# Performance work log

Measured on AMD Instinct MI355X. Metric: run time of the kernel, lower is better.

## Reference

```python
import jax, jax.numpy as jnp
import numpy as np

N = 50000
H = 8
D = 32
E = 400000
IN = 128
NEG_SLOPE = 0.2


def _gat(h, edges, W, al, ar, b):
    # DGL GATConv: fc -> per-head attention logits -> edge softmax over dst -> aggregate
    src, dst = edges[0], edges[1]
    feat = (h @ W).reshape(N, H, D)                      # [N,H,D]
    el = jnp.einsum('nhd,hd->nh', feat, al)              # [N,H]
    er = jnp.einsum('nhd,hd->nh', feat, ar)              # [N,H]
    e = jax.nn.leaky_relu(el[src] + er[dst], NEG_SLOPE)  # [E,H]
    m = jax.ops.segment_max(e, dst, num_segments=N)      # [N,H] per-dst max
    m = jnp.where(jnp.isfinite(m), m, 0.0)
    m = jax.lax.stop_gradient(m)
    ex = jnp.exp(e - m[dst])                             # [E,H]
    denom = jax.ops.segment_sum(ex, dst, num_segments=N) # [N,H]
    alpha = ex / denom[dst]                              # edge softmax
    out = jax.ops.segment_sum(feat[src] * alpha[:, :, None], dst, num_segments=N)  # [N,H,D]
    return (out + b.reshape(1, H, D)).reshape(N, H * D)


def setup_inputs() -> dict:
    key = jax.random.key(0)
    ks = jax.random.split(key, 12)
    s = 0.05
    return {
        'h': jax.random.normal(ks[0], (N, IN), jnp.float32),
        'edges0': jax.random.randint(ks[1], (2, E), 0, N, jnp.int32),
        'edges1': jax.random.randint(ks[2], (2, E), 0, N, jnp.int32),
        'fc0': jax.random.normal(ks[3], (IN, H * D), jnp.float32) * s,
        'al0': jax.random.normal(ks[4], (H, D), jnp.float32) * s,
        'ar0': jax.random.normal(ks[5], (H, D), jnp.float32) * s,
        'bias0': jnp.zeros((H * D,), jnp.float32),
        'fc1': jax.random.normal(ks[6], (IN, H * D), jnp.float32) * s,
        'al1': jax.random.normal(ks[7], (H, D), jnp.float32) * s,
        'ar1': jax.random.normal(ks[8], (H, D), jnp.float32) * s,
        'bias1': jnp.zeros((H * D,), jnp.float32),
        'sw1': jax.random.normal(ks[9], (H * D, 128), jnp.float32) * s,
        'sb1': jnp.zeros((128,), jnp.float32),
        'sw2': jax.random.normal(ks[10], (128, 1), jnp.float32) * s,
    }


def reference(h, edges0, edges1, fc0, al0, ar0, bias0, fc1, al1, ar1, bias1, sw1, sb1, sw2):
    z0 = _gat(h, edges0, fc0, al0, ar0, bias0)   # [N, H*D]
    z1 = _gat(h, edges1, fc1, al1, ar1, bias1)   # [N, H*D]
    z = jnp.stack([z0, z1], axis=1)              # [N, M=2, H*D]
    # semantic attention: MLP -> mean over nodes -> softmax over meta-paths
    w = jnp.tanh(z @ sw1 + sb1) @ sw2            # [N,M,1]
    beta = jax.nn.softmax(w.mean(axis=0), axis=0)  # [M,1]
    return (beta[None] * z).sum(axis=1)          # [N, H*D]
```

## Files before the change

kernel.cpp:

```cpp
#include <hip/hip_runtime.h>
#include <math.h>

#define NEG_SLOPE 0.2f

typedef unsigned int uint;
typedef unsigned short ushort;
typedef __bf16 bf16x8 __attribute__((ext_vector_type(8)));
typedef float f32x4 __attribute__((ext_vector_type(4)));

__device__ __forceinline__ uint bf16r(float a) {
    uint u = __float_as_uint(a);
    return (u + 0x7fffu + ((u >> 16) & 1u)) >> 16;
}
__device__ __forceinline__ uint bf16pack(float a, float b) {
    return bf16r(a) | (bf16r(b) << 16);
}
__device__ __forceinline__ float bflo(uint u) { return __uint_as_float(u << 16); }
__device__ __forceinline__ float bfhi(uint u) { return __uint_as_float(u & 0xffff0000u); }

__global__ void prep_kernel(const float* __restrict__ fc0, const float* __restrict__ fc1,
                            const float* __restrict__ sw1, ushort* __restrict__ wbt,
                            ushort* __restrict__ sw1t, float* __restrict__ wsum) {
    int b = blockIdx.x;
    if (b == 0 && threadIdx.x == 0) { wsum[0] = 0.f; wsum[1] = 0.f; }
    if (b < 256) {
        int idx = b * 256 + threadIdx.x;
        const float* W = (idx >> 15) ? fc1 : fc0;
        int r = idx & 32767;
        int c = r >> 7, k = r & 127;
        wbt[idx] = (ushort)bf16r(W[(size_t)k * 256 + c]);
    } else {
        int idx = (b - 256) * 256 + threadIdx.x;
        int c = idx >> 8, p = idx & 255;
        int col = (p & ~63) + ((p & 3) * 16) + ((p >> 2) & 15);
        sw1t[idx] = (ushort)bf16r(sw1[(size_t)col * 128 + c]);
    }
}

__global__ void zero_counts_kernel(int* __restrict__ count, int* __restrict__ cursor, int Ntot) {
    int i = blockIdx.x * blockDim.x + threadIdx.x;
    if (i < Ntot) { count[i] = 0; cursor[i] = 0; }
}

__global__ void hist_kernel(const int* __restrict__ e0, const int* __restrict__ e1,
                            int* __restrict__ count, int E, int N) {
    int e = blockIdx.x * blockDim.x + threadIdx.x;
    if (e >= 2 * E) return;
    int l = (e >= E);
    int ee = e - l * E;
    const int* edges = l ? e1 : e0;
    atomicAdd(&count[edges[E + ee] + l * N], 1);
}

__global__ void scan1_kernel(const int* __restrict__ count, int* __restrict__ base,
                             int* __restrict__ bsum, int Ntot) {
    __shared__ int ws_s[4];
    int b = blockIdx.x;
    int i = b * 256 + threadIdx.x;
    int v = (i < Ntot) ? count[i] : 0;
    int lane = threadIdx.x & 63;
    int wid = threadIdx.x >> 6;
    int x = v;
#pragma unroll
    for (int s = 1; s < 64; s <<= 1) {
        int y = __shfl_up(x, s, 64);
        if (lane >= s) x += y;
    }
    if (lane == 63) ws_s[wid] = x;
    __syncthreads();
    int add = 0;
    for (int w = 0; w < wid; w++) add += ws_s[w];
    int incl = x + add;
    if (i < Ntot) base[i] = incl - v;
    if (threadIdx.x == 255) bsum[b] = incl;
}

__global__ void scan2_kernel(int* __restrict__ bsum, int nb) {
    __shared__ int ws_s[4];
    __shared__ int running_s;
    if (threadIdx.x == 0) running_s = 0;
    __syncthreads();
    int lane = threadIdx.x & 63;
    int wid = threadIdx.x >> 6;
    for (int c0 = 0; c0 < nb; c0 += 256) {
        int i = c0 + threadIdx.x;
        int v = (i < nb) ? bsum[i] : 0;
        int x = v;
#pragma unroll
        for (int s = 1; s < 64; s <<= 1) {
            int y = __shfl_up(x, s, 64);
            if (lane >= s) x += y;
        }
        if (lane == 63) ws_s[wid] = x;
        __syncthreads();
        int add = 0;
        for (int w = 0; w < wid; w++) add += ws_s[w];
        int incl = x + add;
        int run = running_s;
        if (i < nb) bsum[i] = run + incl - v;
        __syncthreads();
        if (threadIdx.x == 255) running_s = run + incl;
        __syncthreads();
    }
}

#define HKPAD 136
__global__ void __launch_bounds__(256, 4)
fc_kernel(const float* __restrict__ h, const ushort* __restrict__ wbt,
          const float* __restrict__ al0, const float* __restrict__ ar0,
          const float* __restrict__ al1, const float* __restrict__ ar1,
          ushort* __restrict__ featb, float* __restrict__ el,
          float* __restrict__ er, int N, int nb) {
    __shared__ ushort hs[64 * HKPAD];
    int b = blockIdx.x;
    int l = (b >= nb);
    int n0 = (b - l * nb) * 64;
    for (int t = threadIdx.x; t < 64 * 32; t += 256) {
        int r = t >> 5, i4 = t & 31;
        int n = n0 + r;
        float4 v = make_float4(0.f, 0.f, 0.f, 0.f);
        if (n < N) v = ((const float4*)h)[(size_t)n * 32 + i4];
        uint2 pk;
        pk.x = bf16pack(v.x, v.y);
        pk.y = bf16pack(v.z, v.w);
        *((uint2*)(hs + r * HKPAD + i4 * 4)) = pk;
    }
    __syncthreads();

    const ushort* wb = wbt + l * 32768;
    const float* al = l ? al1 : al0;
    const float* ar = l ? ar1 : ar0;
    ushort* fb = featb + (size_t)l * N * 256;
    float* elp = el + (size_t)l * N * 8;
    float* erp = er + (size_t)l * N * 8;

    int wv = threadIdx.x >> 6;
    int lane = threadIdx.x & 63;
    int lhi = lane >> 4, llo = lane & 15;

    f32x4 acc[4][4];
#pragma unroll
    for (int cb = 0; cb < 4; cb++)
#pragma unroll
        for (int rt = 0; rt < 4; rt++) acc[cb][rt] = (f32x4){0.f, 0.f, 0.f, 0.f};

#pragma unroll
    for (int ks = 0; ks < 4; ks++) {
        bf16x8 a[4];
#pragma unroll
        for (int rt = 0; rt < 4; rt++)
            a[rt] = *(const bf16x8*)(hs + (rt * 16 + llo) * HKPAD + ks * 32 + lhi * 8);
#pragma unroll
        for (int cb = 0; cb < 4; cb++) {
            bf16x8 bfrag = *(const bf16x8*)(wb + (size_t)(64 * wv + 16 * cb + llo) * 128 + ks * 32 + lhi * 8);
#pragma unroll
            for (int rt = 0; rt < 4; rt++)
                acc[cb][rt] = __builtin_amdgcn_mfma_f32_16x16x32_bf16(a[rt], bfrag, acc[cb][rt], 0, 0, 0);
        }
    }

    float alv0 = al[64 * wv + llo],      alv1 = al[64 * wv + 16 + llo];
    float alv2 = al[64 * wv + 32 + llo], alv3 = al[64 * wv + 48 + llo];
    float arv0 = ar[64 * wv + llo],      arv1 = ar[64 * wv + 16 + llo];
    float arv2 = ar[64 * wv + 32 + llo], arv3 = ar[64 * wv + 48 + llo];

#pragma unroll
    for (int rt = 0; rt < 4; rt++) {
#pragma unroll
        for (int reg = 0; reg < 4; reg++) {
            int n = n0 + rt * 16 + lhi * 4 + reg;
            bool valid = (n < N);
            uint2 pv;
            pv.x = bf16pack(acc[0][rt][reg], acc[1][rt][reg]);
            pv.y = bf16pack(acc[2][rt][reg], acc[3][rt][reg]);
            if (valid) *((uint2*)(fb + (size_t)n * 256 + 64 * wv + 4 * llo)) = pv;
            float pl0 = acc[0][rt][reg] * alv0 + acc[1][rt][reg] * alv1;
            float pl1 = acc[2][rt][reg] * alv2 + acc[3][rt][reg] * alv3;
            float pr0 = acc[0][rt][reg] * arv0 + acc[1][rt][reg] * arv1;
            float pr1 = acc[2][rt][reg] * arv2 + acc[3][rt][reg] * arv3;
#pragma unroll
            for (int s = 1; s <= 8; s <<= 1) {
                pl0 += __shfl_xor(pl0, s, 64);
                pl1 += __shfl_xor(pl1, s, 64);
                pr0 += __shfl_xor(pr0, s, 64);
                pr1 += __shfl_xor(pr1, s, 64);
            }
            if (llo == 0 && valid) {
                *((float2*)(elp + (size_t)n * 8 + 2 * wv)) = make_float2(pl0, pl1);
                *((float2*)(erp + (size_t)n * 8 + 2 * wv)) = make_float2(pr0, pr1);
            }
        }
    }
}

__global__ void scatter_kernel(const int* __restrict__ e0, const int* __restrict__ e1,
                               const float* __restrict__ el, const float* __restrict__ er,
                               const int* __restrict__ base, const int* __restrict__ bsum,
                               int* __restrict__ cursor, int* __restrict__ csr_src,
                               float* __restrict__ pedge, int E, int N) {
    int e = blockIdx.x * blockDim.x + threadIdx.x;
    if (e >= 2 * E) return;
    int l = (e >= E);
    int ee = e - l * E;
    const int* edges = l ? e1 : e0;
    int src = edges[ee];
    int dst = edges[E + ee];
    int d = dst + l * N;
    int pos = base[d] + bsum[d >> 8] + atomicAdd(&cursor[d], 1);
    csr_src[pos] = src;
    size_t so = (size_t)(l * N + src) * 2;
    size_t dofs = (size_t)(l * N + dst) * 2;
    float4 l0 = ((const float4*)el)[so];
    float4 l1 = ((const float4*)el)[so + 1];
    float4 r0 = ((const float4*)er)[dofs];
    float4 r1 = ((const float4*)er)[dofs + 1];
    float v[8] = {l0.x + r0.x, l0.y + r0.y, l0.z + r0.z, l0.w + r0.w,
                  l1.x + r1.x, l1.y + r1.y, l1.z + r1.z, l1.w + r1.w};
#pragma unroll
    for (int k = 0; k < 8; k++) {
        float t = (v[k] > 0.f) ? v[k] : NEG_SLOPE * v[k];
        v[k] = __expf(t);
    }
    ((float4*)pedge)[pos * 2]     = make_float4(v[0], v[1], v[2], v[3]);
    ((float4*)pedge)[pos * 2 + 1] = make_float4(v[4], v[5], v[6], v[7]);
}

__global__ void aggregate_csr_kernel(const int* __restrict__ csr_src, const float* __restrict__ pedge,
                                     const int* __restrict__ base, const int* __restrict__ bsum,
                                     const int* __restrict__ count, const ushort* __restrict__ featb,
                                     const float* __restrict__ bias0, const float* __restrict__ bias1,
                                     ushort* __restrict__ z0b, ushort* __restrict__ z1b, int N) {
    int wid = threadIdx.x >> 6;
    int lane = threadIdx.x & 63;
    int d = blockIdx.x * 4 + wid;
    if (d >= 2 * N) return;
    int l = (d >= N);
    int dst = d - l * N;
    int row0 = base[d] + bsum[d >> 8];
    int deg = count[d];
    int w = lane >> 4, llo = lane & 15;
    const ushort* fb = featb + (size_t)l * N * 256;
    const float2* pe = (const float2*)(pedge + (size_t)row0 * 8);
    const int* cs = csr_src + row0;
    const uint2* fb2 = (const uint2*)fb;

    float d0 = 0.f, d1 = 0.f;
    float4 a = make_float4(0.f, 0.f, 0.f, 0.f);
    int t = 0;
    for (; t + 4 <= deg; t += 4) {
        int s0 = cs[t], s1 = cs[t + 1], s2 = cs[t + 2], s3 = cs[t + 3];
        float2 q0 = pe[t * 4 + w];
        float2 q1 = pe[t * 4 + 4 + w];
        float2 q2 = pe[t * 4 + 8 + w];
        float2 q3 = pe[t * 4 + 12 + w];
        uint2 u0 = fb2[(size_t)s0 * 64 + lane];
        uint2 u1 = fb2[(size_t)s1 * 64 + lane];
        uint2 u2 = fb2[(size_t)s2 * 64 + lane];
        uint2 u3 = fb2[(size_t)s3 * 64 + lane];
        d0 += q0.x; d1 += q0.y;
        a.x += q0.x * bflo(u0.x); a.y += q0.x * bfhi(u0.x);
        a.z += q0.y * bflo(u0.y); a.w += q0.y * bfhi(u0.y);
        d0 += q1.x; d1 += q1.y;
        a.x += q1.x * bflo(u1.x); a.y += q1.x * bfhi(u1.x);
        a.z += q1.y * bflo(u1.y); a.w += q1.y * bfhi(u1.y);
        d0 += q2.x; d1 += q2.y;
        a.x += q2.x * bflo(u2.x); a.y += q2.x * bfhi(u2.x);
        a.z += q2.y * bflo(u2.y); a.w += q2.y * bfhi(u2.y);
        d0 += q3.x; d1 += q3.y;
        a.x += q3.x * bflo(u3.x); a.y += q3.x * bfhi(u3.x);
        a.z += q3.y * bflo(u3.y); a.w += q3.y * bfhi(u3.y);
    }
    for (; t < deg; t++) {
        int s0 = cs[t];
        float2 q0 = pe[t * 4 + w];
        uint2 u0 = fb2[(size_t)s0 * 64 + lane];
        d0 += q0.x; d1 += q0.y;
        a.x += q0.x * bflo(u0.x); a.y += q0.x * bfhi(u0.x);
        a.z += q0.y * bflo(u0.y); a.w += q0.y * bfhi(u0.y);
    }
    const float* bias = l ? bias1 : bias0;
    int c0 = 64 * w + llo;
    float b0 = bias[c0], b1 = bias[c0 + 16], b2 = bias[c0 + 32], b3 = bias[c0 + 48];
    float i0 = (d0 > 0.f) ? 1.f / d0 : 0.f;
    float i1 = (d1 > 0.f) ? 1.f / d1 : 0.f;
    uint2 o;
    o.x = bf16pack(a.x * i0 + b0, a.y * i0 + b1);
    o.y = bf16pack(a.z * i1 + b2, a.w * i1 + b3);
    ushort* zb = l ? z1b : z0b;
    ((uint2*)zb)[(size_t)dst * 64 + lane] = o;
}

#define ZROW 264
__global__ void __launch_bounds__(256, 4)
semantic_kernel(const ushort* __restrict__ z0b, const ushort* __restrict__ z1b,
                const ushort* __restrict__ sw1t, const float* __restrict__ sb1,
                const float* __restrict__ sw2, float* __restrict__ wsum, int N) {
    __shared__ ushort zs[64 * ZROW];
    __shared__ float rowp[64];
    int n0 = blockIdx.x * 32;
    if (threadIdx.x < 64) rowp[threadIdx.x] = 0.f;
    for (int t = threadIdx.x; t < 64 * 32; t += 256) {
        int row = t >> 5, i16 = t & 31;
        int r = row >> 1, mm = row & 1;
        int n = n0 + r;
        uint4 v = make_uint4(0u, 0u, 0u, 0u);
        if (n < N) v = ((const uint4*)(mm ? z1b : z0b))[(size_t)n * 32 + i16];
        *((uint4*)(zs + row * ZROW + i16 * 8)) = v;
    }
    __syncthreads();

    int wv = threadIdx.x >> 6;
    int lane = threadIdx.x & 63;
    int lhi = lane >> 4, llo = lane & 15;

    f32x4 acc[2][4];
#pragma unroll
    for (int c = 0; c < 2; c++)
#pragma unroll
        for (int rt = 0; rt < 4; rt++) acc[c][rt] = (f32x4){0.f, 0.f, 0.f, 0.f};

#pragma unroll
    for (int ks = 0; ks < 8; ks++) {
        bf16x8 b0 = *(const bf16x8*)(sw1t + (size_t)((2 * wv) * 16 + llo) * 256 + ks * 32 + lhi * 8);
        bf16x8 b1 = *(const bf16x8*)(sw1t + (size_t)((2 * wv + 1) * 16 + llo) * 256 + ks * 32 + lhi * 8);
#pragma unroll
        for (int rt = 0; rt < 4; rt++) {
            bf16x8 av = *(const bf16x8*)(zs + (rt * 16 + llo) * ZROW + ks * 32 + lhi * 8);
            acc[0][rt] = __builtin_amdgcn_mfma_f32_16x16x32_bf16(av, b0, acc[0][rt], 0, 0, 0);
            acc[1][rt] = __builtin_amdgcn_mfma_f32_16x16x32_bf16(av, b1, acc[1][rt], 0, 0, 0);
        }
    }

    float sb0 = sb1[(2 * wv) * 16 + llo],      s20 = sw2[(2 * wv) * 16 + llo];
    float sb1v = sb1[(2 * wv + 1) * 16 + llo], s21 = sw2[(2 * wv + 1) * 16 + llo];
#pragma unroll
    for (int rt = 0; rt < 4; rt++) {
        float pr[4];
#pragma unroll
        for (int reg = 0; reg < 4; reg++)
            pr[reg] = tanhf(acc[0][rt][reg] + sb0) * s20 + tanhf(acc[1][rt][reg] + sb1v) * s21;
#pragma unroll
        for (int s = 1; s <= 8; s <<= 1)
#pragma unroll
            for (int reg = 0; reg < 4; reg++) pr[reg] += __shfl_xor(pr[reg], s, 64);
        if (llo == 0) {
#pragma unroll
            for (int reg = 0; reg < 4; reg++)
                atomicAdd(&rowp[rt * 16 + lhi * 4 + reg], pr[reg]);
        }
    }
    __syncthreads();
    if (threadIdx.x < 64) {
        int node = n0 + (threadIdx.x >> 1);
        float v = (node < N) ? rowp[threadIdx.x] : 0.f;
        v += __shfl_xor(v, 2, 64);
        v += __shfl_xor(v, 4, 64);
        v += __shfl_xor(v, 8, 64);
        v += __shfl_xor(v, 16, 64);
        v += __shfl_xor(v, 32, 64);
        if (threadIdx.x < 2) atomicAdd(&wsum[threadIdx.x], v);
    }
}

__global__ void beta_kernel(const float* __restrict__ wsum, float* __restrict__ beta, float invN) {
    if (threadIdx.x == 0 && blockIdx.x == 0) {
        float w0 = wsum[0] * invN, w1 = wsum[1] * invN;
        float mx = fmaxf(w0, w1);
        float e0 = expf(w0 - mx), e1 = expf(w1 - mx);
        float s = e0 + e1;
        beta[0] = e0 / s;
        beta[1] = e1 / s;
    }
}

__global__ void combine_kernel(float* __restrict__ out, const ushort* __restrict__ z0b,
                               const ushort* __restrict__ z1b, const float* __restrict__ beta,
                               int N) {
    int idx = blockIdx.x * 256 + threadIdx.x;
    if (idx >= N * 64) return;
    int n = idx >> 6, lane = idx & 63;
    int w = lane >> 4, llo = lane & 15;
    float b0 = beta[0], b1 = beta[1];
    uint2 a = ((const uint2*)z0b)[idx];
    uint2 b = ((const uint2*)z1b)[idx];
    float* o = out + (size_t)n * 256 + 64 * w + llo;
    o[0]  = b0 * bflo(a.x) + b1 * bflo(b.x);
    o[16] = b0 * bfhi(a.x) + b1 * bfhi(b.x);
    o[32] = b0 * bflo(a.y) + b1 * bflo(b.y);
    o[48] = b0 * bfhi(a.y) + b1 * bfhi(b.y);
}

extern "C" void kernel_launch(void* const* d_in, const int* in_sizes, int n_in,
                              void* d_out, int out_size, void* d_ws, size_t ws_size,
                              hipStream_t stream) {
    const float* h      = (const float*)d_in[0];
    const int*   edges0 = (const int*)d_in[1];
    const int*   edges1 = (const int*)d_in[2];
    const float* fc0    = (const float*)d_in[3];
    const float* al0    = (const float*)d_in[4];
    const float* ar0    = (const float*)d_in[5];
    const float* bias0  = (const float*)d_in[6];
    const float* fc1    = (const float*)d_in[7];
    const float* al1    = (const float*)d_in[8];
    const float* ar1    = (const float*)d_in[9];
    const float* bias1  = (const float*)d_in[10];
    const float* sw1    = (const float*)d_in[11];
    const float* sb1    = (const float*)d_in[12];
    const float* sw2    = (const float*)d_in[13];

    const int N = in_sizes[0] / 128;
    const int E = in_sizes[1] / 2;
    const int Ntot = 2 * N;
    const int NB2 = (Ntot + 255) / 256;
    const int nb = (N + 63) / 64;

    char* ws = (char*)d_ws;
    ushort* featb = (ushort*)ws;
    ushort* z0b   = featb + (size_t)Ntot * 256;
    ushort* z1b   = z0b + (size_t)N * 256;
    ushort* wbt   = z1b + (size_t)N * 256;
    ushort* sw1t  = wbt + 2 * 256 * 128;
    float*  el    = (float*)(sw1t + 128 * 256);
    float*  er    = el + (size_t)Ntot * 8;
    float*  pedge = er + (size_t)Ntot * 8;
    int*    csr_src = (int*)(pedge + (size_t)E * 16);
    int*    count   = csr_src + 2 * E;
    int*    base    = count + Ntot;
    int*    cursor  = base + Ntot;
    int*    bsum    = cursor + Ntot;
    float*  wsum  = (float*)(bsum + NB2 + 2);
    float*  beta  = wsum + 2;
    float*  outp  = (float*)d_out;

    prep_kernel<<<384, 256, 0, stream>>>(fc0, fc1, sw1, wbt, sw1t, wsum);
    zero_counts_kernel<<<NB2, 256, 0, stream>>>(count, cursor, Ntot);
    hist_kernel<<<(2 * E + 255) / 256, 256, 0, stream>>>(edges0, edges1, count, E, N);
    scan1_kernel<<<NB2, 256, 0, stream>>>(count, base, bsum, Ntot);
    scan2_kernel<<<1, 256, 0, stream>>>(bsum, NB2);
    fc_kernel<<<2 * nb, 256, 0, stream>>>(h, wbt, al0, ar0, al1, ar1, featb, el, er, N, nb);
    scatter_kernel<<<(2 * E + 255) / 256, 256, 0, stream>>>(edges0, edges1, el, er, base, bsum,
                                                            cursor, csr_src, pedge, E, N);
    aggregate_csr_kernel<<<(Ntot + 3) / 4, 256, 0, stream>>>(csr_src, pedge, base, bsum, count,
                                                             featb, bias0, bias1, z0b, z1b, N);
    semantic_kernel<<<(N + 31) / 32, 256, 0, stream>>>(z0b, z1b, sw1t, sb1, sw2, wsum, N);
    beta_kernel<<<1, 64, 0, stream>>>(wsum, beta, 1.0f / (float)N);
    combine_kernel<<<(N * 64 + 255) / 256, 256, 0, stream>>>(outp, z0b, z1b, beta, N);
}
```

Measured before the change: 264.9 us.

## Compute edge attention inside CSR aggregation and fold small kernels into neighbors

Edge logits are no longer computed and stored per edge in the scatter kernel. The aggregation kernel now recomputes leaky-relu and exp on the fly from el[src] and er[dst], using two waves per destination node with one head per lane pair and scalar source indices via readfirstlane. The count/cursor zeroing moves into prep_kernel, and beta_kernel is removed by computing the semantic softmax inside combine_kernel. This drops the pedge buffer's write and read traffic and two launches, but adds an exp per lane per edge, a scattered el gather, and halves the feature width handled per wave.

```diff
diff --git a/kernel.cpp b/kernel.cpp
--- a/kernel.cpp
+++ b/kernel.cpp
@@ -20,7 +20,8 @@
 
 __global__ void prep_kernel(const float* __restrict__ fc0, const float* __restrict__ fc1,
                             const float* __restrict__ sw1, ushort* __restrict__ wbt,
-                            ushort* __restrict__ sw1t, float* __restrict__ wsum) {
+                            ushort* __restrict__ sw1t, float* __restrict__ wsum,
+                            int* __restrict__ count, int* __restrict__ cursor, int Ntot) {
     int b = blockIdx.x;
     if (b == 0 && threadIdx.x == 0) { wsum[0] = 0.f; wsum[1] = 0.f; }
     if (b < 256) {
@@ -29,17 +30,15 @@
         int r = idx & 32767;
         int c = r >> 7, k = r & 127;
         wbt[idx] = (ushort)bf16r(W[(size_t)k * 256 + c]);
-    } else {
+    } else if (b < 384) {
         int idx = (b - 256) * 256 + threadIdx.x;
         int c = idx >> 8, p = idx & 255;
         int col = (p & ~63) + ((p & 3) * 16) + ((p >> 2) & 15);
         sw1t[idx] = (ushort)bf16r(sw1[(size_t)col * 128 + c]);
-    }
-}
-
-__global__ void zero_counts_kernel(int* __restrict__ count, int* __restrict__ cursor, int Ntot) {
-    int i = blockIdx.x * blockDim.x + threadIdx.x;
-    if (i < Ntot) { count[i] = 0; cursor[i] = 0; }
+    } else {
+        int i = (b - 384) * 256 + threadIdx.x;
+        if (i < Ntot) { count[i] = 0; cursor[i] = 0; }
+    }
 }
 
 __global__ void hist_kernel(const int* __restrict__ e0, const int* __restrict__ e1,
@@ -194,10 +193,9 @@
 }
 
 __global__ void scatter_kernel(const int* __restrict__ e0, const int* __restrict__ e1,
-                               const float* __restrict__ el, const float* __restrict__ er,
                                const int* __restrict__ base, const int* __restrict__ bsum,
                                int* __restrict__ cursor, int* __restrict__ csr_src,
-                               float* __restrict__ pedge, int E, int N) {
+                               int E, int N) {
     int e = blockIdx.x * blockDim.x + threadIdx.x;
     if (e >= 2 * E) return;
     int l = (e >= E);
@@ -208,86 +206,71 @@
     int d = dst + l * N;
     int pos = base[d] + bsum[d >> 8] + atomicAdd(&cursor[d], 1);
     csr_src[pos] = src;
-    size_t so = (size_t)(l * N + src) * 2;
-    size_t dofs = (size_t)(l * N + dst) * 2;
-    float4 l0 = ((const float4*)el)[so];
-    float4 l1 = ((const float4*)el)[so + 1];
-    float4 r0 = ((const float4*)er)[dofs];
-    float4 r1 = ((const float4*)er)[dofs + 1];
-    float v[8] = {l0.x + r0.x, l0.y + r0.y, l0.z + r0.z, l0.w + r0.w,
-                  l1.x + r1.x, l1.y + r1.y, l1.z + r1.z, l1.w + r1.w};
-#pragma unroll
-    for (int k = 0; k < 8; k++) {
-        float t = (v[k] > 0.f) ? v[k] : NEG_SLOPE * v[k];
-        v[k] = __expf(t);
-    }
-    ((float4*)pedge)[pos * 2]     = make_float4(v[0], v[1], v[2], v[3]);
-    ((float4*)pedge)[pos * 2 + 1] = make_float4(v[4], v[5], v[6], v[7]);
-}
-
-__global__ void aggregate_csr_kernel(const int* __restrict__ csr_src, const float* __restrict__ pedge,
-                                     const int* __restrict__ base, const int* __restrict__ bsum,
-                                     const int* __restrict__ count, const ushort* __restrict__ featb,
+}
+
+__global__ void aggregate_csr_kernel(const int* __restrict__ csr_src, const float* __restrict__ el,
+                                     const float* __restrict__ er, const int* __restrict__ base,
+                                     const int* __restrict__ bsum, const int* __restrict__ count,
+                                     const ushort* __restrict__ featb,
                                      const float* __restrict__ bias0, const float* __restrict__ bias1,
                                      ushort* __restrict__ z0b, ushort* __restrict__ z1b, int N) {
     int wid = threadIdx.x >> 6;
     int lane = threadIdx.x & 63;
-    int d = blockIdx.x * 4 + wid;
-    if (d >= 2 * N) return;
+    int gw = blockIdx.x * 4 + wid;
+    if (gw >= 4 * N) return;
+    int d = gw >> 1, half = gw & 1;
     int l = (d >= N);
     int dst = d - l * N;
     int row0 = base[d] + bsum[d >> 8];
     int deg = count[d];
-    int w = lane >> 4, llo = lane & 15;
-    const ushort* fb = featb + (size_t)l * N * 256;
-    const float2* pe = (const float2*)(pedge + (size_t)row0 * 8);
+    int hh = 4 * half + ((lane >> 5) << 1) + (lane & 1);
+    int p0 = half * 128 + 2 * lane;
+    int p1 = p0 + 1;
+    int c0 = 64 * (p0 >> 6) + 16 * (p0 & 3) + ((p0 >> 2) & 15);
+    int c1 = 64 * (p1 >> 6) + 16 * (p1 & 3) + ((p1 >> 2) & 15);
+
+    const float* elb = el + (size_t)l * N * 8;
+    float erv = er[((size_t)l * N + dst) * 8 + hh];
+    const uint* fbu = ((const uint*)featb) + (size_t)l * N * 128;
     const int* cs = csr_src + row0;
-    const uint2* fb2 = (const uint2*)fb;
-
-    float d0 = 0.f, d1 = 0.f;
-    float4 a = make_float4(0.f, 0.f, 0.f, 0.f);
+    int lo = half * 64 + lane;
+
+    float dacc = 0.f, a0 = 0.f, a1 = 0.f;
     int t = 0;
     for (; t + 4 <= deg; t += 4) {
-        int s0 = cs[t], s1 = cs[t + 1], s2 = cs[t + 2], s3 = cs[t + 3];
-        float2 q0 = pe[t * 4 + w];
-        float2 q1 = pe[t * 4 + 4 + w];
-        float2 q2 = pe[t * 4 + 8 + w];
-        float2 q3 = pe[t * 4 + 12 + w];
-        uint2 u0 = fb2[(size_t)s0 * 64 + lane];
-        uint2 u1 = fb2[(size_t)s1 * 64 + lane];
-        uint2 u2 = fb2[(size_t)s2 * 64 + lane];
-        uint2 u3 = fb2[(size_t)s3 * 64 + lane];
-        d0 += q0.x; d1 += q0.y;
-        a.x += q0.x * bflo(u0.x); a.y += q0.x * bfhi(u0.x);
-        a.z += q0.y * bflo(u0.y); a.w += q0.y * bfhi(u0.y);
-        d0 += q1.x; d1 += q1.y;
-        a.x += q1.x * bflo(u1.x); a.y += q1.x * bfhi(u1.x);
-        a.z += q1.y * bflo(u1.y); a.w += q1.y * bfhi(u1.y);
-        d0 += q2.x; d1 += q2.y;
-        a.x += q2.x * bflo(u2.x); a.y += q2.x * bfhi(u2.x);
-        a.z += q2.y * bflo(u2.y); a.w += q2.y * bfhi(u2.y);
-        d0 += q3.x; d1 += q3.y;
-        a.x += q3.x * bflo(u3.x); a.y += q3.x * bfhi(u3.x);
-        a.z += q3.y * bflo(u3.y); a.w += q3.y * bfhi(u3.y);
+        int s0 = __builtin_amdgcn_readfirstlane(cs[t]);
+        int s1 = __builtin_amdgcn_readfirstlane(cs[t + 1]);
+        int s2 = __builtin_amdgcn_readfirstlane(cs[t + 2]);
+        int s3 = __builtin_amdgcn_readfirstlane(cs[t + 3]);
+        float x0 = elb[(size_t)s0 * 8 + hh] + erv;
+        float x1 = elb[(size_t)s1 * 8 + hh] + erv;
+        float x2 = elb[(size_t)s2 * 8 + hh] + erv;
+        float x3 = elb[(size_t)s3 * 8 + hh] + erv;
+        uint u0 = fbu[(size_t)s0 * 128 + lo];
+        uint u1 = fbu[(size_t)s1 * 128 + lo];
+        uint u2 = fbu[(size_t)s2 * 128 + lo];
+        uint u3 = fbu[(size_t)s3 * 128 + lo];
+        x0 = (x0 > 0.f) ? x0 : NEG_SLOPE * x0;  float q0 = __expf(x0);
+        x1 = (x1 > 0.f) ? x1 : NEG_SLOPE * x1;  float q1 = __expf(x1);
+        x2 = (x2 > 0.f) ? x2 : NEG_SLOPE * x2;  float q2 = __expf(x2);
+        x3 = (x3 > 0.f) ? x3 : NEG_SLOPE * x3;  float q3 = __expf(x3);
+        dacc += q0; a0 += q0 * bflo(u0); a1 += q0 * bfhi(u0);
+        dacc += q1; a0 += q1 * bflo(u1); a1 += q1 * bfhi(u1);
+        dacc += q2; a0 += q2 * bflo(u2); a1 += q2 * bfhi(u2);
+        dacc += q3; a0 += q3 * bflo(u3); a1 += q3 * bfhi(u3);
     }
     for (; t < deg; t++) {
-        int s0 = cs[t];
-        float2 q0 = pe[t * 4 + w];
-        uint2 u0 = fb2[(size_t)s0 * 64 + lane];
-        d0 += q0.x; d1 += q0.y;
-        a.x += q0.x * bflo(u0.x); a.y += q0.x * bfhi(u0.x);
-        a.z += q0.y * bflo(u0.y); a.w += q0.y * bfhi(u0.y);
+        int s0 = __builtin_amdgcn_readfirstlane(cs[t]);
+        float x0 = elb[(size_t)s0 * 8 + hh] + erv;
+        uint u0 = fbu[(size_t)s0 * 128 + lo];
+        x0 = (x0 > 0.f) ? x0 : NEG_SLOPE * x0;  float q0 = __expf(x0);
+        dacc += q0; a0 += q0 * bflo(u0); a1 += q0 * bfhi(u0);
     }
     const float* bias = l ? bias1 : bias0;
-    int c0 = 64 * w + llo;
-    float b0 = bias[c0], b1 = bias[c0 + 16], b2 = bias[c0 + 32], b3 = bias[c0 + 48];
-    float i0 = (d0 > 0.f) ? 1.f / d0 : 0.f;
-    float i1 = (d1 > 0.f) ? 1.f / d1 : 0.f;
-    uint2 o;
-    o.x = bf16pack(a.x * i0 + b0, a.y * i0 + b1);
-    o.y = bf16pack(a.z * i1 + b2, a.w * i1 + b3);
-    ushort* zb = l ? z1b : z0b;
-    ((uint2*)zb)[(size_t)dst * 64 + lane] = o;
+    float inv = (dacc > 0.f) ? 1.f / dacc : 0.f;
+    uint o = bf16pack(a0 * inv + bias[c0], a1 * inv + bias[c1]);
+    uint* zb = (uint*)(l ? z1b : z0b);
+    zb[(size_t)dst * 128 + lo] = o;
 }
 
 #define ZROW 264
@@ -362,25 +345,17 @@
     }
 }
 
-__global__ void beta_kernel(const float* __restrict__ wsum, float* __restrict__ beta, float invN) {
-    if (threadIdx.x == 0 && blockIdx.x == 0) {
-        float w0 = wsum[0] * invN, w1 = wsum[1] * invN;
-        float mx = fmaxf(w0, w1);
-        float e0 = expf(w0 - mx), e1 = expf(w1 - mx);
-        float s = e0 + e1;
-        beta[0] = e0 / s;
-        beta[1] = e1 / s;
-    }
-}
-
 __global__ void combine_kernel(float* __restrict__ out, const ushort* __restrict__ z0b,
-                               const ushort* __restrict__ z1b, const float* __restrict__ beta,
-                               int N) {
+                               const ushort* __restrict__ z1b, const float* __restrict__ wsum,
+                               float invN, int N) {
     int idx = blockIdx.x * 256 + threadIdx.x;
     if (idx >= N * 64) return;
+    float w0 = wsum[0] * invN, w1 = wsum[1] * invN;
+    float mx = fmaxf(w0, w1);
+    float e0 = __expf(w0 - mx), e1 = __expf(w1 - mx);
+    float b0 = e0 / (e0 + e1), b1 = e1 / (e0 + e1);
     int n = idx >> 6, lane = idx & 63;
     int w = lane >> 4, llo = lane & 15;
-    float b0 = beta[0], b1 = beta[1];
     uint2 a = ((const uint2*)z0b)[idx];
     uint2 b = ((const uint2*)z1b)[idx];
     float* o = out + (size_t)n * 256 + 64 * w + llo;
@@ -422,27 +397,25 @@
     ushort* sw1t  = wbt + 2 * 256 * 128;
     float*  el    = (float*)(sw1t + 128 * 256);
     float*  er    = el + (size_t)Ntot * 8;
-    float*  pedge = er + (size_t)Ntot * 8;
-    int*    csr_src = (int*)(pedge + (size_t)E * 16);
+    int*    csr_src = (int*)(er + (size_t)Ntot * 8);
     int*    count   = csr_src + 2 * E;
     int*    base    = count + Ntot;
     int*    cursor  = base + Ntot;
     int*    bsum    = cursor + Ntot;
     float*  wsum  = (float*)(bsum + NB2 + 2);
-    float*  beta  = wsum + 2;
     float*  outp  = (float*)d_out;
 
-    prep_kernel<<<384, 256, 0, stream>>>(fc0, fc1, sw1, wbt, sw1t, wsum);
-    zero_counts_kernel<<<NB2, 256, 0, stream>>>(count, cursor, Ntot);
+    prep_kernel<<<384 + NB2, 256, 0, stream>>>(fc0, fc1, sw1, wbt, sw1t, wsum,
+                                               count, cursor, Ntot);
     hist_kernel<<<(2 * E + 255) / 256, 256, 0, stream>>>(edges0, edges1, count, E, N);
     scan1_kernel<<<NB2, 256, 0, stream>>>(count, base, bsum, Ntot);
     scan2_kernel<<<1, 256, 0, stream>>>(bsum, NB2);
     fc_kernel<<<2 * nb, 256, 0, stream>>>(h, wbt, al0, ar0, al1, ar1, featb, el, er, N, nb);
-    scatter_kernel<<<(2 * E + 255) / 256, 256, 0, stream>>>(edges0, edges1, el, er, base, bsum,
-                                                            cursor, csr_src, pedge, E, N);
-    aggregate_csr_kernel<<<(Ntot + 3) / 4, 256, 0, stream>>>(csr_src, pedge, base, bsum, count,
-                                                             featb, bias0, bias1, z0b, z1b, N);
+    scatter_kernel<<<(2 * E + 255) / 256, 256, 0, stream>>>(edges0, edges1, base, bsum,
+                                                            cursor, csr_src, E, N);
+    aggregate_csr_kernel<<<N, 256, 0, stream>>>(csr_src, el, er, base, bsum, count,
+                                                featb, bias0, bias1, z0b, z1b, N);
     semantic_kernel<<<(N + 31) / 32, 256, 0, stream>>>(z0b, z1b, sw1t, sb1, sw2, wsum, N);
-    beta_kernel<<<1, 64, 0, stream>>>(wsum, beta, 1.0f / (float)N);
-    combine_kernel<<<(N * 64 + 255) / 256, 256, 0, stream>>>(outp, z0b, z1b, beta, N);
-}
+    combine_kernel<<<(N * 64 + 255) / 256, 256, 0, stream>>>(outp, z0b, z1b, wsum,
+                                                             1.0f / (float)N, N);
+}
```

Result: slower. 287.5 us (+8.5%).
